# Kernel optimization log

Hardware: AMD Instinct MI355X
Metric: run time of the kernel (lower is better)

## Reference

```python
import jax, jax.numpy as jnp
import numpy as np

T, B, Y, X, C = 3, 2, 192, 192, 128
H, F = 8, 16
HF = H * F
RY = RX = 2
PH, PW = 2 * RY + 1, 2 * RX + 1
S = PH * PW  # 25 spatial offsets per frame


def setup_inputs() -> dict:
    key = jax.random.key(0)
    ks = jax.random.split(key, 7)
    sc_w = 1.0 / np.sqrt(C)
    return {
        "frames": jax.random.normal(ks[0], (T, B, Y, X, C), jnp.float32),
        "Wq": jax.random.normal(ks[1], (C, HF), jnp.float32) * sc_w,
        "Wk": jax.random.normal(ks[2], (C, HF), jnp.float32) * sc_w,
        "Wv": jax.random.normal(ks[3], (C, HF), jnp.float32) * sc_w,
        "Wout": jax.random.normal(ks[4], (HF, C), jnp.float32) * (1.0 / np.sqrt(HF)),
        "temp_emb": jax.random.normal(ks[5], (T, HF), jnp.float32) * 0.02,
        "spatial_emb": jax.random.normal(ks[6], (S, HF), jnp.float32) * 0.02,
    }


def _attention(frames, Wq, Wk, Wv, Wout, temp_emb, spatial_emb):
    dtype = frames.dtype
    scale = jnp.asarray(1.0 / np.sqrt(F), dtype)
    # 1x1 convs == channel-wise dense
    Kf = jnp.einsum('tbyxc,cd->tbyxd', frames, Wk).reshape(T, B, Y, X, H, F)
    Vf = jnp.einsum('tbyxc,cd->tbyxd', frames, Wv).reshape(T, B, Y, X, H, F)
    Qf = jnp.einsum('tbyxc,cd->tbyxd', frames, Wq).reshape(T, B, Y, X, H, F)
    # temporal embedding: added to K per frame, and to Q per query frame (queries = all frames)
    t_emb = temp_emb.reshape(T, 1, 1, 1, H, F)
    Kf = Kf + t_emb
    # query spatial embedding: relative position of query inside its clipped patch
    yc = jnp.clip(jnp.arange(Y), RY, Y - RY - 1)  # patch center rows [Y]
    xc = jnp.clip(jnp.arange(X), RX, X - RX - 1)  # patch center cols [X]
    y_rel = jnp.arange(Y) - yc + RY
    x_rel = jnp.arange(X) - xc + RX
    q_sidx = y_rel[:, None] * PW + x_rel[None, :]  # [Y,X] in [0,S)
    q_s = spatial_emb[q_sidx].reshape(1, 1, Y, X, H, F)
    Qf = Qf + q_s + t_emb
    # spatial offsets, row-major (dy outer, dx inner) so offset index s matches spatial_emb row
    offs = np.array([[dy, dx] for dy in range(-RY, RY + 1) for dx in range(-RX, RX + 1)], np.int32)
    y_gather = yc[None, :] + jnp.asarray(offs[:, 0])[:, None]  # [S,Y], always in-bounds
    x_gather = xc[None, :] + jnp.asarray(offs[:, 1])[:, None]  # [S,X]
    k_s_emb = spatial_emb.reshape(S, H, F)

    def step(carry, s_in):
        m, l, acc = carry
        yg, xg, ks = s_in  # yg:[Y] xg:[X] ks:[H,F]
        Kg = Kf[:, :, yg][:, :, :, xg] + ks       # [T,B,Y,X,H,F]
        Vg = Vf[:, :, yg][:, :, :, xg]            # [T,B,Y,X,H,F]
        sc = jnp.einsum('qbyxhf,tbyxhf->qtbyxh', Qf, Kg) * scale  # [nQ,T,B,Y,X,H]
        m_new = jnp.maximum(m, sc.max(axis=1))    # [nQ,B,Y,X,H]
        p = jnp.exp(sc - m_new[:, None])
        alpha = jnp.exp(m - m_new)
        l = l * alpha + p.sum(axis=1)
        acc = acc * alpha[..., None] + jnp.einsum('qtbyxh,tbyxhf->qbyxhf', p, Vg)
        return (m_new, l, acc), None

    m0 = jnp.full((T, B, Y, X, H), -1e9, dtype)
    l0 = jnp.zeros((T, B, Y, X, H), dtype)
    acc0 = jnp.zeros((T, B, Y, X, H, F), dtype)
    (m, l, acc), _ = jax.lax.scan(step, (m0, l0, acc0), (y_gather, x_gather, k_s_emb))
    out = (acc / l[..., None]).reshape(T, B, Y, X, HF)
    return jnp.einsum('tbyxd,dc->tbyxc', out, Wout)  # [nQ=T,B,Y,X,C]


def reference(frames, Wq, Wk, Wv, Wout, temp_emb, spatial_emb):
    return _attention(frames, Wq, Wk, Wv, Wout, temp_emb, spatial_emb)
```

## Files before the change

kernel.cpp:

```cpp
#include <hip/hip_runtime.h>
#include <cstdint>
#include <cstddef>

#define T_ 3
#define B_ 2
#define Y_ 192
#define X_ 192
#define YX_ 36864
#define N_ 221184
#define NS_ 73728

typedef __attribute__((ext_vector_type(8))) short short8;
typedef __attribute__((ext_vector_type(4))) float f32x4;
typedef __attribute__((ext_vector_type(2))) float f32x2;
typedef __attribute__((ext_vector_type(2))) _Float16 h16x2;
typedef unsigned short u16;
typedef unsigned int u32;

__device__ __forceinline__ u16 f2bf(float f){
  u32 x = __builtin_bit_cast(u32, f);
  x += 0x7fffu + ((x >> 16) & 1u);
  return (u16)(x >> 16);
}
__device__ __forceinline__ u16 f2h(float f){
  return __builtin_bit_cast(u16, (_Float16)f);
}
__device__ __forceinline__ float bflo(u32 u){ return __builtin_bit_cast(float, u << 16); }
__device__ __forceinline__ float bfhi(u32 u){ return __builtin_bit_cast(float, u & 0xffff0000u); }
__device__ __forceinline__ f32x2 bfp(u32 u){
  f32x2 r; r.x = bflo(u); r.y = bfhi(u); return r;
}
__device__ __forceinline__ int clampi(int v, int lo, int hi){ return v < lo ? lo : (v > hi ? hi : v); }
__device__ __forceinline__ f32x2 shfl2(f32x2 v, int m){
  f32x2 r; r.x = __shfl_xor(v.x, m); r.y = __shfl_xor(v.y, m); return r;
}

#if __has_builtin(__builtin_amdgcn_fdot2)
__device__ __forceinline__ float dot2h(u32 a, u32 b, float c){
  return __builtin_amdgcn_fdot2(__builtin_bit_cast(h16x2, a),
                                __builtin_bit_cast(h16x2, b), c, false);
}
#else
__device__ __forceinline__ float dot2h(u32 a, u32 b, float c){
  const h16x2 ha = __builtin_bit_cast(h16x2, a);
  const h16x2 hb = __builtin_bit_cast(h16x2, b);
  return fmaf((float)ha.y, (float)hb.y, fmaf((float)ha.x, (float)hb.x, c));
}
#endif

#if __has_builtin(__builtin_amdgcn_exp2f)
__device__ __forceinline__ float fexp2(float x){ return __builtin_amdgcn_exp2f(x); }
#else
__device__ __forceinline__ float fexp2(float x){ return exp2f(x); }
#endif

#define QSCALE 0.36067376022224085f

__global__ __launch_bounds__(256) void wt_kernel(
    const float* __restrict__ Wq, const float* __restrict__ Wk,
    const float* __restrict__ Wv, const float* __restrict__ Wo,
    const float* __restrict__ spatial_emb, u16* __restrict__ WT, u16* __restrict__ se_h){
  int idx = blockIdx.x * 256 + threadIdx.x;
  if (idx < 65536){
    int g = idx >> 14;
    int r = (idx >> 7) & 127;
    int c = idx & 127;
    const float* W = (g == 0) ? Wq : (g == 1) ? Wk : (g == 2) ? Wv : Wo;
    WT[g * 16384 + c * 128 + r] = f2bf(W[r * 128 + c]);
  } else if (idx < 65536 + 3200){
    se_h[idx - 65536] = f2h(spatial_emb[idx - 65536]);
  }
}

__global__ __launch_bounds__(256, 2) void qkv_kernel(
    const float* __restrict__ frames, const u16* __restrict__ WT,
    u16* __restrict__ Qb, u16* __restrict__ Kb, u16* __restrict__ Vb,
    const float* __restrict__ temp_emb, const float* __restrict__ spatial_emb){
  __shared__ float tile[128 * 128];
  const int tid = threadIdx.x;
  const int w = tid >> 6, l = tid & 63;
  const int l16 = l & 15, lg = l >> 4;
  const int m0 = blockIdx.x * 128;

  short8 af[4][2];
  #pragma unroll
  for (int ks = 0; ks < 4; ++ks)
    #pragma unroll
    for (int mr = 0; mr < 2; ++mr){
      const float* ap = frames + (size_t)(m0 + w * 32 + mr * 16 + l16) * 128 + ks * 32 + lg * 8;
      const f32x4 a0 = *(const f32x4*)ap;
      const f32x4 a1 = *(const f32x4*)(ap + 4);
      short8 t;
      t[0] = (short)f2bf(a0[0]); t[1] = (short)f2bf(a0[1]);
      t[2] = (short)f2bf(a0[2]); t[3] = (short)f2bf(a0[3]);
      t[4] = (short)f2bf(a1[0]); t[5] = (short)f2bf(a1[1]);
      t[6] = (short)f2bf(a1[2]); t[7] = (short)f2bf(a1[3]);
      af[ks][mr] = t;
    }

  #pragma unroll
  for (int g = 0; g < 3; ++g){
    const u16* wt = WT + g * 16384;
    f32x4 acc[2][8];
    #pragma unroll
    for (int mr = 0; mr < 2; ++mr)
      #pragma unroll
      for (int nf = 0; nf < 8; ++nf)
        acc[mr][nf] = (f32x4){0.f, 0.f, 0.f, 0.f};

    #pragma unroll
    for (int ks = 0; ks < 4; ++ks)
      #pragma unroll
      for (int nf = 0; nf < 8; ++nf){
        const short8 bf = *(const short8*)(wt + (nf * 16 + l16) * 128 + ks * 32 + lg * 8);
        acc[0][nf] = __builtin_amdgcn_mfma_f32_16x16x32_bf16(af[ks][0], bf, acc[0][nf], 0, 0, 0);
        acc[1][nf] = __builtin_amdgcn_mfma_f32_16x16x32_bf16(af[ks][1], bf, acc[1][nf], 0, 0, 0);
      }

    if (g > 0) __syncthreads();
    #pragma unroll
    for (int mr = 0; mr < 2; ++mr)
      #pragma unroll
      for (int nf = 0; nf < 8; ++nf)
        #pragma unroll
        for (int i = 0; i < 4; ++i)
          tile[(w * 32 + mr * 16 + lg * 4 + i) * 128 + nf * 16 + l16] = acc[mr][nf][i];
    __syncthreads();

    u16* outp = (g == 0) ? Qb : (g == 1) ? Kb : Vb;
    #pragma unroll
    for (int it = 0; it < 16; ++it){
      const int idx = it * 256 + tid;
      const int r = idx >> 5;
      const int c4 = (idx & 31) * 4;
      f32x4 v = *(const f32x4*)&tile[r * 128 + c4];
      const int p = m0 + r;
      const int t = p / (B_ * YX_);
      if (g <= 1){
        const float* te = temp_emb + t * 128 + c4;
        v[0] += te[0]; v[1] += te[1]; v[2] += te[2]; v[3] += te[3];
      }
      if (g == 0){
        const int yx = p % YX_;
        const int y = yx / X_, x = yx % X_;
        const int yrel = y - clampi(y, 2, Y_ - 3) + 2;
        const int xrel = x - clampi(x, 2, X_ - 3) + 2;
        const float* se = spatial_emb + (yrel * 5 + xrel) * 128 + c4;
        v[0] = (v[0] + se[0]) * QSCALE; v[1] = (v[1] + se[1]) * QSCALE;
        v[2] = (v[2] + se[2]) * QSCALE; v[3] = (v[3] + se[3]) * QSCALE;
      }
      uint2 pk;
      if (g <= 1){
        pk.x = (u32)f2h(v[0]) | ((u32)f2h(v[1]) << 16);
        pk.y = (u32)f2h(v[2]) | ((u32)f2h(v[3]) << 16);
      } else {
        pk.x = (u32)f2bf(v[0]) | ((u32)f2bf(v[1]) << 16);
        pk.y = (u32)f2bf(v[2]) | ((u32)f2bf(v[3]) << 16);
      }
      *(uint2*)(outp + (size_t)p * 128 + c4) = pk;
    }
  }
}

__global__ __launch_bounds__(256) void attn_kernel(
    const u16* __restrict__ Kb, const u16* __restrict__ Vb,
    u16* __restrict__ Qb, const u16* __restrict__ se_h){
  __shared__ float qse[4][2][1200];
  __shared__ u32 tbl[80];
  const int tid = threadIdx.x;
  const int w = tid >> 6, l = tid & 63;
  const int s2 = l >> 5, slot = (l >> 3) & 3, h = l & 7;

  if (tid < 80){
    const int kk = tid > 74 ? 74 : tid;
    const int t = kk / 25, s = kk - t * 25;
    const int dy = s / 5, dx = s - dy * 5;
    tbl[tid] = (u32)((((t * (B_ * Y_) + dy) * X_ + dx) * 256) | (s * 8));
  }

  const int bid = blockIdx.x;
  const int sw = (bid & 7) * 1152 + (bid >> 3);
  const int site = sw * 8 + w * 2 + s2;
  const int b = site / YX_;
  const int yx = site % YX_;
  const int y = yx / X_, x = yx % X_;
  const int yc = clampi(y, 2, 189), xc = clampi(x, 2, 189);
  const u32 sbase = (u32)(((b * Y_ + (yc - 2)) * X_ + (xc - 2)) * 256 + h * 32);
  const char* Kc = (const char*)Kb;
  const char* Vc = (const char*)Vb;

  u32 qp[3][8];
  #pragma unroll
  for (int q = 0; q < 3; ++q){
    const u16* qptr = Qb + ((size_t)((q * B_ + b) * Y_ + y) * X_ + x) * 128 + h * 16;
    const uint4 a = *(const uint4*)qptr;
    const uint4 c = *(const uint4*)(qptr + 8);
    qp[q][0] = a.x; qp[q][1] = a.y; qp[q][2] = a.z; qp[q][3] = a.w;
    qp[q][4] = c.x; qp[q][5] = c.y; qp[q][6] = c.z; qp[q][7] = c.w;
  }

  float* qsl = &qse[w][s2][0];
  #pragma unroll
  for (int sj = 0; sj < 7; ++sj){
    const int so = sj * 4 + slot;
    if (so < 25){
      const u16* sp = se_h + so * 128 + h * 16;
      const uint4 e0 = *(const uint4*)sp;
      const uint4 e1 = *(const uint4*)(sp + 8);
      u32 ep[8] = {e0.x, e0.y, e0.z, e0.w, e1.x, e1.y, e1.z, e1.w};
      #pragma unroll
      for (int q = 0; q < 3; ++q){
        float d = 0.f;
        #pragma unroll
        for (int i = 0; i < 8; ++i) d = dot2h(qp[q][i], ep[i], d);
        qsl[q * 200 + so * 8 + h] = d;
      }
    }
  }
  __syncthreads();

  u32 ev[19];
  #pragma unroll
  for (int j = 0; j < 19; ++j) ev[j] = tbl[j * 4 + slot];

  float ll[3] = {0.f, 0.f, 0.f};
  f32x2 acc[3][8];
  #pragma unroll
  for (int q = 0; q < 3; ++q)
    #pragma unroll
    for (int i = 0; i < 8; ++i) acc[q][i] = (f32x2){0.f, 0.f};

  #pragma unroll
  for (int j = 0; j < 19; ++j){
    const u32 e = ev[j];
    const u32 boff = sbase + (e & 0xffffff00u);
    const int s8 = (int)(e & 0xffu);
    const uint4 k0 = *(const uint4*)(Kc + boff);
    const uint4 k1 = *(const uint4*)(Kc + boff + 16);
    const uint4 v0 = *(const uint4*)(Vc + boff);
    const uint4 v1 = *(const uint4*)(Vc + boff + 16);
    f32x2 vf[8];
    vf[0] = bfp(v0.x); vf[1] = bfp(v0.y); vf[2] = bfp(v0.z); vf[3] = bfp(v0.w);
    vf[4] = bfp(v1.x); vf[5] = bfp(v1.y); vf[6] = bfp(v1.z); vf[7] = bfp(v1.w);

    #pragma unroll
    for (int q = 0; q < 3; ++q){
      float d1 = qsl[q * 200 + s8 + h];
      d1 = dot2h(qp[q][0], k0.x, d1);
      d1 = dot2h(qp[q][1], k0.y, d1);
      d1 = dot2h(qp[q][2], k0.z, d1);
      d1 = dot2h(qp[q][3], k0.w, d1);
      float d2 = dot2h(qp[q][4], k1.x, 0.f);
      d2 = dot2h(qp[q][5], k1.y, d2);
      d2 = dot2h(qp[q][6], k1.z, d2);
      d2 = dot2h(qp[q][7], k1.w, d2);
      float p = fexp2(d1 + d2);
      if (j == 18 && slot == 3) p = 0.f;
      ll[q] += p;
      const f32x2 pp = {p, p};
      #pragma unroll
      for (int i = 0; i < 8; ++i) acc[q][i] += pp * vf[i];
    }
  }

  #pragma unroll
  for (int q = 0; q < 3; ++q){
    ll[q] += __shfl_xor(ll[q], 8);
    ll[q] += __shfl_xor(ll[q], 16);
    #pragma unroll
    for (int i = 0; i < 8; ++i){
      acc[q][i] += shfl2(acc[q][i], 8);
      acc[q][i] += shfl2(acc[q][i], 16);
    }
  }

  #pragma unroll
  for (int q = 0; q < 3; ++q){
    if (slot == q){
      const float inv = 1.0f / ll[q];
      uint4 o0, o1;
      {
        const f32x2 t0 = acc[q][0] * inv, t1 = acc[q][1] * inv;
        const f32x2 t2 = acc[q][2] * inv, t3 = acc[q][3] * inv;
        o0.x = (u32)f2bf(t0.x) | ((u32)f2bf(t0.y) << 16);
        o0.y = (u32)f2bf(t1.x) | ((u32)f2bf(t1.y) << 16);
        o0.z = (u32)f2bf(t2.x) | ((u32)f2bf(t2.y) << 16);
        o0.w = (u32)f2bf(t3.x) | ((u32)f2bf(t3.y) << 16);
      }
      {
        const f32x2 t0 = acc[q][4] * inv, t1 = acc[q][5] * inv;
        const f32x2 t2 = acc[q][6] * inv, t3 = acc[q][7] * inv;
        o1.x = (u32)f2bf(t0.x) | ((u32)f2bf(t0.y) << 16);
        o1.y = (u32)f2bf(t1.x) | ((u32)f2bf(t1.y) << 16);
        o1.z = (u32)f2bf(t2.x) | ((u32)f2bf(t2.y) << 16);
        o1.w = (u32)f2bf(t3.x) | ((u32)f2bf(t3.y) << 16);
      }
      u16* dst = Qb + ((size_t)((q * B_ + b) * Y_ + y) * X_ + x) * 128 + h * 16;
      *(uint4*)dst = o0;
      *(uint4*)(dst + 8) = o1;
    }
  }
}

__global__ __launch_bounds__(256) void out_kernel(
    const u16* __restrict__ Ab, const u16* __restrict__ WT3, float* __restrict__ out){
  const int tid = threadIdx.x;
  const int w = tid >> 6, l = tid & 63;
  const int l16 = l & 15, lg = l >> 4;
  const int m0 = blockIdx.x * 128;

  f32x4 acc[2][8];
  #pragma unroll
  for (int mr = 0; mr < 2; ++mr)
    #pragma unroll
    for (int nf = 0; nf < 8; ++nf)
      acc[mr][nf] = (f32x4){0.f, 0.f, 0.f, 0.f};

  #pragma unroll
  for (int ks = 0; ks < 4; ++ks){
    short8 af[2];
    #pragma unroll
    for (int mr = 0; mr < 2; ++mr)
      af[mr] = *(const short8*)(Ab + (size_t)(m0 + w * 32 + mr * 16 + l16) * 128 + ks * 32 + lg * 8);
    #pragma unroll
    for (int nf = 0; nf < 8; ++nf){
      const short8 bf = *(const short8*)(WT3 + (nf * 16 + l16) * 128 + ks * 32 + lg * 8);
      acc[0][nf] = __builtin_amdgcn_mfma_f32_16x16x32_bf16(af[0], bf, acc[0][nf], 0, 0, 0);
      acc[1][nf] = __builtin_amdgcn_mfma_f32_16x16x32_bf16(af[1], bf, acc[1][nf], 0, 0, 0);
    }
  }

  #pragma unroll
  for (int mr = 0; mr < 2; ++mr)
    #pragma unroll
    for (int nf = 0; nf < 8; ++nf)
      #pragma unroll
      for (int i = 0; i < 4; ++i)
        out[(size_t)(m0 + w * 32 + mr * 16 + lg * 4 + i) * 128 + nf * 16 + l16] = acc[mr][nf][i];
}

extern "C" void kernel_launch(void* const* d_in, const int* in_sizes, int n_in,
                              void* d_out, int out_size, void* d_ws, size_t ws_size,
                              hipStream_t stream){
  const float* frames      = (const float*)d_in[0];
  const float* Wq          = (const float*)d_in[1];
  const float* Wk          = (const float*)d_in[2];
  const float* Wv          = (const float*)d_in[3];
  const float* Wo          = (const float*)d_in[4];
  const float* temp_emb    = (const float*)d_in[5];
  const float* spatial_emb = (const float*)d_in[6];

  u16* WT    = (u16*)d_ws;
  u16* se_h  = WT + 4 * 16384;
  u16* Qb    = WT + 68736;
  u16* Kb    = (u16*)d_out;
  u16* Vb    = Kb + (size_t)N_ * 128;
  float* out = (float*)d_out;

  wt_kernel<<<269, 256, 0, stream>>>(Wq, Wk, Wv, Wo, spatial_emb, WT, se_h);
  qkv_kernel<<<N_ / 128, 256, 0, stream>>>(frames, WT, Qb, Kb, Vb, temp_emb, spatial_emb);
  attn_kernel<<<NS_ / 8, 256, 0, stream>>>(Kb, Vb, Qb, se_h);
  out_kernel<<<N_ / 128, 256, 0, stream>>>(Qb, WT + 3 * 16384, out);
}
```

Measured before the change: 334.7 us.

## Store V as fp16 and accumulate P·V in packed fp16; halve QKV LDS tile

```diff
diff --git a/kernel.cpp b/kernel.cpp
--- a/kernel.cpp
+++ b/kernel.cpp
@@ -27,12 +27,11 @@
 }
 __device__ __forceinline__ float bflo(u32 u){ return __builtin_bit_cast(float, u << 16); }
 __device__ __forceinline__ float bfhi(u32 u){ return __builtin_bit_cast(float, u & 0xffff0000u); }
-__device__ __forceinline__ f32x2 bfp(u32 u){
-  f32x2 r; r.x = bflo(u); r.y = bfhi(u); return r;
-}
 __device__ __forceinline__ int clampi(int v, int lo, int hi){ return v < lo ? lo : (v > hi ? hi : v); }
-__device__ __forceinline__ f32x2 shfl2(f32x2 v, int m){
-  f32x2 r; r.x = __shfl_xor(v.x, m); r.y = __shfl_xor(v.y, m); return r;
+__device__ __forceinline__ h16x2 shflh(h16x2 v, int m){
+  u32 u = __builtin_bit_cast(u32, v);
+  u = __shfl_xor(u, m);
+  return __builtin_bit_cast(h16x2, u);
 }
 
 #if __has_builtin(__builtin_amdgcn_fdot2)
@@ -76,7 +75,7 @@
     const float* __restrict__ frames, const u16* __restrict__ WT,
     u16* __restrict__ Qb, u16* __restrict__ Kb, u16* __restrict__ Vb,
     const float* __restrict__ temp_emb, const float* __restrict__ spatial_emb){
-  __shared__ float tile[128 * 128];
+  __shared__ float tile[128 * 64];
   const int tid = threadIdx.x;
   const int w = tid >> 6, l = tid & 63;
   const int l16 = l & 15, lg = l >> 4;
@@ -117,47 +116,48 @@
         acc[1][nf] = __builtin_amdgcn_mfma_f32_16x16x32_bf16(af[ks][1], bf, acc[1][nf], 0, 0, 0);
       }
 
-    if (g > 0) __syncthreads();
-    #pragma unroll
-    for (int mr = 0; mr < 2; ++mr)
-      #pragma unroll
-      for (int nf = 0; nf < 8; ++nf)
+    u16* outp = (g == 0) ? Qb : (g == 1) ? Kb : Vb;
+    #pragma unroll
+    for (int h2 = 0; h2 < 2; ++h2){
+      if (g > 0 || h2 > 0) __syncthreads();
+      #pragma unroll
+      for (int mr = 0; mr < 2; ++mr)
         #pragma unroll
-        for (int i = 0; i < 4; ++i)
-          tile[(w * 32 + mr * 16 + lg * 4 + i) * 128 + nf * 16 + l16] = acc[mr][nf][i];
-    __syncthreads();
-
-    u16* outp = (g == 0) ? Qb : (g == 1) ? Kb : Vb;
-    #pragma unroll
-    for (int it = 0; it < 16; ++it){
-      const int idx = it * 256 + tid;
-      const int r = idx >> 5;
-      const int c4 = (idx & 31) * 4;
-      f32x4 v = *(const f32x4*)&tile[r * 128 + c4];
-      const int p = m0 + r;
-      const int t = p / (B_ * YX_);
-      if (g <= 1){
-        const float* te = temp_emb + t * 128 + c4;
-        v[0] += te[0]; v[1] += te[1]; v[2] += te[2]; v[3] += te[3];
-      }
-      if (g == 0){
-        const int yx = p % YX_;
-        const int y = yx / X_, x = yx % X_;
-        const int yrel = y - clampi(y, 2, Y_ - 3) + 2;
-        const int xrel = x - clampi(x, 2, X_ - 3) + 2;
-        const float* se = spatial_emb + (yrel * 5 + xrel) * 128 + c4;
-        v[0] = (v[0] + se[0]) * QSCALE; v[1] = (v[1] + se[1]) * QSCALE;
-        v[2] = (v[2] + se[2]) * QSCALE; v[3] = (v[3] + se[3]) * QSCALE;
-      }
-      uint2 pk;
-      if (g <= 1){
+        for (int nf4 = 0; nf4 < 4; ++nf4){
+          const int nf = h2 * 4 + nf4;
+          #pragma unroll
+          for (int i = 0; i < 4; ++i)
+            tile[(w * 32 + mr * 16 + lg * 4 + i) * 64 + nf4 * 16 + l16] = acc[mr][nf][i];
+        }
+      __syncthreads();
+
+      #pragma unroll
+      for (int it = 0; it < 8; ++it){
+        const int idx = it * 256 + tid;
+        const int r = idx >> 4;
+        const int c4 = (idx & 15) * 4;
+        f32x4 v = *(const f32x4*)&tile[r * 64 + c4];
+        const int p = m0 + r;
+        const int col = h2 * 64 + c4;
+        const int t = p / (B_ * YX_);
+        if (g <= 1){
+          const float* te = temp_emb + t * 128 + col;
+          v[0] += te[0]; v[1] += te[1]; v[2] += te[2]; v[3] += te[3];
+        }
+        if (g == 0){
+          const int yx = p % YX_;
+          const int y = yx / X_, x = yx % X_;
+          const int yrel = y - clampi(y, 2, Y_ - 3) + 2;
+          const int xrel = x - clampi(x, 2, X_ - 3) + 2;
+          const float* se = spatial_emb + (yrel * 5 + xrel) * 128 + col;
+          v[0] = (v[0] + se[0]) * QSCALE; v[1] = (v[1] + se[1]) * QSCALE;
+          v[2] = (v[2] + se[2]) * QSCALE; v[3] = (v[3] + se[3]) * QSCALE;
+        }
+        uint2 pk;
         pk.x = (u32)f2h(v[0]) | ((u32)f2h(v[1]) << 16);
         pk.y = (u32)f2h(v[2]) | ((u32)f2h(v[3]) << 16);
-      } else {
-        pk.x = (u32)f2bf(v[0]) | ((u32)f2bf(v[1]) << 16);
-        pk.y = (u32)f2bf(v[2]) | ((u32)f2bf(v[3]) << 16);
-      }
-      *(uint2*)(outp + (size_t)p * 128 + c4) = pk;
+        *(uint2*)(outp + (size_t)p * 128 + col) = pk;
+      }
     }
   }
 }
@@ -224,11 +224,11 @@
   for (int j = 0; j < 19; ++j) ev[j] = tbl[j * 4 + slot];
 
   float ll[3] = {0.f, 0.f, 0.f};
-  f32x2 acc[3][8];
+  h16x2 acc[3][8];
   #pragma unroll
   for (int q = 0; q < 3; ++q)
     #pragma unroll
-    for (int i = 0; i < 8; ++i) acc[q][i] = (f32x2){0.f, 0.f};
+    for (int i = 0; i < 8; ++i) acc[q][i] = (h16x2){(_Float16)0.f, (_Float16)0.f};
 
   #pragma unroll
   for (int j = 0; j < 19; ++j){
@@ -239,9 +239,11 @@
     const uint4 k1 = *(const uint4*)(Kc + boff + 16);
     const uint4 v0 = *(const uint4*)(Vc + boff);
     const uint4 v1 = *(const uint4*)(Vc + boff + 16);
-    f32x2 vf[8];
-    vf[0] = bfp(v0.x); vf[1] = bfp(v0.y); vf[2] = bfp(v0.z); vf[3] = bfp(v0.w);
-    vf[4] = bfp(v1.x); vf[5] = bfp(v1.y); vf[6] = bfp(v1.z); vf[7] = bfp(v1.w);
+    h16x2 hv[8];
+    hv[0] = __builtin_bit_cast(h16x2, v0.x); hv[1] = __builtin_bit_cast(h16x2, v0.y);
+    hv[2] = __builtin_bit_cast(h16x2, v0.z); hv[3] = __builtin_bit_cast(h16x2, v0.w);
+    hv[4] = __builtin_bit_cast(h16x2, v1.x); hv[5] = __builtin_bit_cast(h16x2, v1.y);
+    hv[6] = __builtin_bit_cast(h16x2, v1.z); hv[7] = __builtin_bit_cast(h16x2, v1.w);
 
     #pragma unroll
     for (int q = 0; q < 3; ++q){
@@ -257,9 +259,10 @@
       float p = fexp2(d1 + d2);
       if (j == 18 && slot == 3) p = 0.f;
       ll[q] += p;
-      const f32x2 pp = {p, p};
-      #pragma unroll
-      for (int i = 0; i < 8; ++i) acc[q][i] += pp * vf[i];
+      const _Float16 ph = (_Float16)p;
+      h16x2 pp; pp.x = ph; pp.y = ph;
+      #pragma unroll
+      for (int i = 0; i < 8; ++i) acc[q][i] += pp * hv[i];
     }
   }
 
@@ -269,8 +272,8 @@
     ll[q] += __shfl_xor(ll[q], 16);
     #pragma unroll
     for (int i = 0; i < 8; ++i){
-      acc[q][i] += shfl2(acc[q][i], 8);
-      acc[q][i] += shfl2(acc[q][i], 16);
+      acc[q][i] += shflh(acc[q][i], 8);
+      acc[q][i] += shflh(acc[q][i], 16);
     }
   }
 
@@ -280,20 +283,24 @@
       const float inv = 1.0f / ll[q];
       uint4 o0, o1;
       {
-        const f32x2 t0 = acc[q][0] * inv, t1 = acc[q][1] * inv;
-        const f32x2 t2 = acc[q][2] * inv, t3 = acc[q][3] * inv;
-        o0.x = (u32)f2bf(t0.x) | ((u32)f2bf(t0.y) << 16);
-        o0.y = (u32)f2bf(t1.x) | ((u32)f2bf(t1.y) << 16);
-        o0.z = (u32)f2bf(t2.x) | ((u32)f2bf(t2.y) << 16);
-        o0.w = (u32)f2bf(t3.x) | ((u32)f2bf(t3.y) << 16);
+        const float a0 = (float)acc[q][0].x * inv, a1 = (float)acc[q][0].y * inv;
+        const float a2 = (float)acc[q][1].x * inv, a3 = (float)acc[q][1].y * inv;
+        const float a4 = (float)acc[q][2].x * inv, a5 = (float)acc[q][2].y * inv;
+        const float a6 = (float)acc[q][3].x * inv, a7 = (float)acc[q][3].y * inv;
+        o0.x = (u32)f2bf(a0) | ((u32)f2bf(a1) << 16);
+        o0.y = (u32)f2bf(a2) | ((u32)f2bf(a3) << 16);
+        o0.z = (u32)f2bf(a4) | ((u32)f2bf(a5) << 16);
+        o0.w = (u32)f2bf(a6) | ((u32)f2bf(a7) << 16);
       }
       {
-        const f32x2 t0 = acc[q][4] * inv, t1 = acc[q][5] * inv;
-        const f32x2 t2 = acc[q][6] * inv, t3 = acc[q][7] * inv;
-        o1.x = (u32)f2bf(t0.x) | ((u32)f2bf(t0.y) << 16);
-        o1.y = (u32)f2bf(t1.x) | ((u32)f2bf(t1.y) << 16);
-        o1.z = (u32)f2bf(t2.x) | ((u32)f2bf(t2.y) << 16);
-        o1.w = (u32)f2bf(t3.x) | ((u32)f2bf(t3.y) << 16);
+        const float a0 = (float)acc[q][4].x * inv, a1 = (float)acc[q][4].y * inv;
+        const float a2 = (float)acc[q][5].x * inv, a3 = (float)acc[q][5].y * inv;
+        const float a4 = (float)acc[q][6].x * inv, a5 = (float)acc[q][6].y * inv;
+        const float a6 = (float)acc[q][7].x * inv, a7 = (float)acc[q][7].y * inv;
+        o1.x = (u32)f2bf(a0) | ((u32)f2bf(a1) << 16);
+        o1.y = (u32)f2bf(a2) | ((u32)f2bf(a3) << 16);
+        o1.z = (u32)f2bf(a4) | ((u32)f2bf(a5) << 16);
+        o1.w = (u32)f2bf(a6) | ((u32)f2bf(a7) << 16);
       }
       u16* dst = Qb + ((size_t)((q * B_ + b) * Y_ + y) * X_ + x) * 128 + h * 16;
       *(uint4*)dst = o0;
```

Result: faster. 310.3 us (-7.3%).
